# Kernel optimization log

Hardware: AMD Instinct MI355X
Metric: run time of the kernel (lower is better)

## Reference

```python
import jax, jax.numpy as jnp
import numpy as np

TEMPERATURE = 0.5
HEAD_DIM = 64
NUM_HEADS = 4

N_NODES = 50000
N_EDGES = 800000
DIM = 256


def setup_inputs() -> dict:
    key = jax.random.key(0)
    ks = jax.random.split(key, 7)
    h = jax.random.normal(ks[0], (N_NODES, DIM), dtype=jnp.float32)
    src = jax.random.randint(ks[1], (N_EDGES,), 0, N_NODES)
    dst = jax.random.randint(ks[2], (N_EDGES,), 0, N_NODES)
    attn_q = jax.random.normal(ks[3], (DIM, NUM_HEADS * HEAD_DIM), dtype=jnp.float32) * 0.02
    attn_k = jax.random.normal(ks[4], (DIM, NUM_HEADS * HEAD_DIM), dtype=jnp.float32) * 0.02
    W = jax.random.normal(ks[5], (DIM, DIM), dtype=jnp.float32) * (1.0 / np.sqrt(DIM))
    b = jnp.zeros((DIM,), dtype=jnp.float32)
    return {"h": h, "src": src, "dst": dst, "attn_q": attn_q, "attn_k": attn_k, "W": W, "b": b}


def _edge_softmax_by_dst(a, dst, n_nodes):
    # softmax over incoming edges of each destination node (DGL edge_softmax)
    m = jax.ops.segment_max(a, dst, num_segments=n_nodes)
    e = jnp.exp(a - m[dst])
    s = jax.ops.segment_sum(e, dst, num_segments=n_nodes)
    return e / s[dst]


def reference(h, src, dst, attn_q, attn_k, W, b):
    n = h.shape[0]
    v = h @ W.T + b                         # iv Linear: [N, D]
    q = h @ attn_q                          # [N, H*64]
    k = h @ attn_k                          # [N, H*64]
    # per-edge score: mean over heads then over head_dim == mean over all H*64,
    # preceded by /8 -> dot(q_src, k_dst) / (8 * H * 64)
    scale = 1.0 / (8.0 * NUM_HEADS * HEAD_DIM)
    a = jnp.einsum('ed,ed->e', q[src], k[dst]) * scale   # [E]
    # global standardization over all edges (std unbiased=False)
    m = a.mean()
    s = jnp.sqrt(((a - m) ** 2).mean())
    a = (a - m) / s / TEMPERATURE
    a = _edge_softmax_by_dst(a, dst, n)     # [E]
    # message passing: sum_{e: dst(e)=i} a_e * v[src(e)]
    out = jax.ops.segment_sum(v[src] * a[:, None], dst, num_segments=n)  # [N, D]
    return out, a
```

## Files before the change

### kernel.cpp

```cpp
#include <hip/hip_runtime.h>
#include <math.h>

#define DIM 256
#define NQKV 768
#define STAT_BLOCKS 2048

typedef float  f32x4 __attribute__((ext_vector_type(4)));
typedef short  bs8   __attribute__((ext_vector_type(8)));

__device__ __forceinline__ ushort f2bf(float f) {
    unsigned int u = __float_as_uint(f);
    u += 0x7fffu + ((u >> 16) & 1u);
    return (ushort)(u >> 16);
}
__device__ __forceinline__ float bf2f(ushort u) {
    return __uint_as_float(((unsigned int)u) << 16);
}

#define MFMA16(c, a, b) \
    asm("s_nop 1\n\tv_mfma_f32_16x16x32_bf16 %0, %1, %2, %0" : "+v"(c) : "v"(a), "v"(b))

__global__ __launch_bounds__(256) void conv_h(
    const float* __restrict__ h, ushort* __restrict__ h_bf, int total8)
{
    const int idx = blockIdx.x * 256 + threadIdx.x;
    if (idx >= total8) return;
    const float4* hp = (const float4*)(h + (size_t)idx * 8);
    float4 a = hp[0], b = hp[1];
    uint4 o;
    o.x = (unsigned)f2bf(a.x) | ((unsigned)f2bf(a.y) << 16);
    o.y = (unsigned)f2bf(a.z) | ((unsigned)f2bf(a.w) << 16);
    o.z = (unsigned)f2bf(b.x) | ((unsigned)f2bf(b.y) << 16);
    o.w = (unsigned)f2bf(b.z) | ((unsigned)f2bf(b.w) << 16);
    *(uint4*)(h_bf + (size_t)idx * 8) = o;
}

__global__ __launch_bounds__(256) void build_bt(
    const float* __restrict__ attn_q, const float* __restrict__ attn_k,
    const float* __restrict__ W, ushort* __restrict__ bt)
{
    const int n = blockIdx.x;
    const int k = threadIdx.x;
    float val;
    if (n < 256)      val = attn_q[(size_t)k * 256 + n];
    else if (n < 512) val = attn_k[(size_t)k * 256 + (n - 256)];
    else              val = W[(size_t)(n - 512) * 256 + k];
    bt[(size_t)n * 256 + k] = f2bf(val);
}

__global__ __launch_bounds__(256) void gemm_qkv_mfma(
    const ushort* __restrict__ h_bf, const ushort* __restrict__ bt,
    const float* __restrict__ bias, ushort* __restrict__ qkv, int M)
{
    __shared__ __align__(16) ushort As[128 * 40];
    __shared__ __align__(16) ushort Bs[128 * 40];

    const int bm = blockIdx.x * 128;
    const int bn = blockIdx.y * 128;
    const int t    = threadIdx.x;
    const int lane = t & 63;
    const int wid  = t >> 6;
    const int wm   = wid >> 1;
    const int wn   = wid & 1;
    const int fr   = lane & 15;
    const int ko   = (lane >> 4) * 8;

    f32x4 acc[4][4];
    #pragma unroll
    for (int i = 0; i < 4; ++i)
        #pragma unroll
        for (int j = 0; j < 4; ++j)
            acc[i][j] = (f32x4){0.f, 0.f, 0.f, 0.f};

    for (int k0 = 0; k0 < DIM; k0 += 32) {
        #pragma unroll
        for (int ii = 0; ii < 2; ++ii) {
            const int s   = t * 2 + ii;
            const int row = s >> 2;
            const int sl  = s & 3;
            int ga = bm + row; if (ga > M - 1) ga = M - 1;
            uint4 va = *(const uint4*)(h_bf + (size_t)ga * 256 + k0 + sl * 8);
            *(uint4*)(As + row * 40 + sl * 8) = va;
            uint4 vb = *(const uint4*)(bt + (size_t)(bn + row) * 256 + k0 + sl * 8);
            *(uint4*)(Bs + row * 40 + sl * 8) = vb;
        }
        __syncthreads();

        bs8 af[4], bf_[4];
        #pragma unroll
        for (int f = 0; f < 4; ++f) {
            af[f]  = *(const bs8*)(As + (wm * 64 + f * 16 + fr) * 40 + ko);
            bf_[f] = *(const bs8*)(Bs + (wn * 64 + f * 16 + fr) * 40 + ko);
        }
        #pragma unroll
        for (int fm = 0; fm < 4; ++fm)
            #pragma unroll
            for (int fn = 0; fn < 4; ++fn)
                MFMA16(acc[fm][fn], af[fm], bf_[fn]);

        __syncthreads();
    }

    asm volatile("s_nop 7\n\ts_nop 7\n\ts_nop 7" ::: );

    #pragma unroll
    for (int fm = 0; fm < 4; ++fm) {
        const int rowbase = bm + wm * 64 + fm * 16 + (lane >> 4) * 4;
        #pragma unroll
        for (int fn = 0; fn < 4; ++fn) {
            const int col = bn + wn * 64 + fn * 16 + fr;
            float bv = (col >= 512) ? bias[col - 512] : 0.f;
            #pragma unroll
            for (int r = 0; r < 4; ++r) {
                const int row = rowbase + r;
                if (row < M)
                    qkv[(size_t)row * NQKV + col] = f2bf(acc[fm][fn][r] + bv);
            }
        }
    }
}

__global__ __launch_bounds__(256) void deg_count(
    const int* __restrict__ dst, int* __restrict__ deg, int E)
{
    const int e = blockIdx.x * 256 + threadIdx.x;
    if (e < E) atomicAdd(&deg[dst[e]], 1);
}

__global__ __launch_bounds__(1024) void scan_rowptr(
    const int* __restrict__ deg, int* __restrict__ row_ptr, int N)
{
    const int tid  = threadIdx.x;
    const int lane = tid & 63;
    const int wv   = tid >> 6;

    if (tid == 0) row_ptr[0] = 0;

    __shared__ int woff[17];
    __shared__ int carryS;
    if (tid == 0) carryS = 0;
    __syncthreads();

    for (int base = 0; base < N; base += 4096) {
        int x[4], pre[4];
        int run = 0;
        #pragma unroll
        for (int j = 0; j < 4; ++j) {
            const int i = base + tid * 4 + j;
            const int v = (i < N) ? deg[i] : 0;
            pre[j] = run; x[j] = v; run += v;
        }
        int incl = run;
        #pragma unroll
        for (int off = 1; off < 64; off <<= 1) {
            int y = __shfl_up(incl, off);
            if (lane >= off) incl += y;
        }
        const int wex = incl - run;
        if (lane == 63) woff[wv] = incl;
        __syncthreads();
        if (wv == 0) {
            int wtot = (lane < 16) ? woff[lane] : 0;
            int winc = wtot;
            #pragma unroll
            for (int off = 1; off < 16; off <<= 1) {
                int y = __shfl_up(winc, off);
                if (lane >= off) winc += y;
            }
            if (lane < 16) woff[lane] = winc - wtot;
            if (lane == 15) woff[16] = winc;
        }
        __syncthreads();
        const int basev = carryS + woff[wv] + wex;
        #pragma unroll
        for (int j = 0; j < 4; ++j) {
            const int i = base + tid * 4 + j;
            if (i < N) row_ptr[i + 1] = basev + pre[j] + x[j];
        }
        __syncthreads();
        if (tid == 0) carryS += woff[16];
        __syncthreads();
    }
}

__global__ __launch_bounds__(256) void scatter_edges(
    const int* __restrict__ src, const int* __restrict__ dst,
    const int* __restrict__ row_ptr, int* __restrict__ cursor,
    int4* __restrict__ edata, int E)
{
    const int e = blockIdx.x * 256 + threadIdx.x;
    if (e < E) {
        const int d = dst[e];
        const int pos = row_ptr[d] + atomicAdd(&cursor[d], 1);
        edata[pos] = make_int4(src[e], d, e, 0);
    }
}

__global__ __launch_bounds__(256) void edge_dot_csr(
    const ushort* __restrict__ qkv, const int4* __restrict__ edata,
    float* __restrict__ a_rawc, double* __restrict__ partials, int E)
{
    const int lane = threadIdx.x & 63;
    const int wid  = threadIdx.x >> 6;
    const int w    = blockIdx.x * 4 + wid;
    const int nw   = gridDim.x * 4;
    const int chunk = (E + nw - 1) / nw;
    const int p0 = w * chunk;
    const int p1 = min(E, p0 + chunk);

    double lsum = 0.0, lsum2 = 0.0;
    int p = p0;
    for (; p + 2 <= p1; p += 2) {
        const int4 e0 = edata[p];
        const int4 e1 = edata[p + 1];
        ushort4 qa0 = *(const ushort4*)(qkv + (size_t)e0.x * NQKV + lane * 4);
        ushort4 kb0 = *(const ushort4*)(qkv + (size_t)e0.y * NQKV + 256 + lane * 4);
        ushort4 qa1 = *(const ushort4*)(qkv + (size_t)e1.x * NQKV + lane * 4);
        ushort4 kb1 = *(const ushort4*)(qkv + (size_t)e1.y * NQKV + 256 + lane * 4);
        float d0 = bf2f(qa0.x) * bf2f(kb0.x) + bf2f(qa0.y) * bf2f(kb0.y)
                 + bf2f(qa0.z) * bf2f(kb0.z) + bf2f(qa0.w) * bf2f(kb0.w);
        float d1 = bf2f(qa1.x) * bf2f(kb1.x) + bf2f(qa1.y) * bf2f(kb1.y)
                 + bf2f(qa1.z) * bf2f(kb1.z) + bf2f(qa1.w) * bf2f(kb1.w);
        #pragma unroll
        for (int off = 32; off; off >>= 1) {
            d0 += __shfl_xor(d0, off);
            d1 += __shfl_xor(d1, off);
        }
        if (lane == 0) {
            a_rawc[p]     = d0;
            a_rawc[p + 1] = d1;
            lsum  += (double)d0 + (double)d1;
            lsum2 += (double)d0 * (double)d0 + (double)d1 * (double)d1;
        }
    }
    if (p < p1) {
        const int4 e0 = edata[p];
        ushort4 qa0 = *(const ushort4*)(qkv + (size_t)e0.x * NQKV + lane * 4);
        ushort4 kb0 = *(const ushort4*)(qkv + (size_t)e0.y * NQKV + 256 + lane * 4);
        float d0 = bf2f(qa0.x) * bf2f(kb0.x) + bf2f(qa0.y) * bf2f(kb0.y)
                 + bf2f(qa0.z) * bf2f(kb0.z) + bf2f(qa0.w) * bf2f(kb0.w);
        #pragma unroll
        for (int off = 32; off; off >>= 1) d0 += __shfl_xor(d0, off);
        if (lane == 0) {
            a_rawc[p] = d0;
            lsum  += (double)d0;
            lsum2 += (double)d0 * (double)d0;
        }
    }

    __shared__ double bsum[4], bsum2[4];
    if (lane == 0) { bsum[wid] = lsum; bsum2[wid] = lsum2; }
    __syncthreads();
    if (threadIdx.x == 0) {
        partials[blockIdx.x]             = bsum[0] + bsum[1] + bsum[2] + bsum[3];
        partials[gridDim.x + blockIdx.x] = bsum2[0] + bsum2[1] + bsum2[2] + bsum2[3];
    }
}

__global__ __launch_bounds__(256) void finalize_coef(
    const double* __restrict__ partials, float* __restrict__ coef, int E)
{
    __shared__ double red[256];
    const int tid = threadIdx.x;
    double s1 = 0.0, s2 = 0.0;
    for (int i = tid; i < STAT_BLOCKS; i += 256) {
        s1 += partials[i];
        s2 += partials[STAT_BLOCKS + i];
    }
    red[tid] = s1;
    __syncthreads();
    for (int off = 128; off; off >>= 1) {
        if (tid < off) red[tid] += red[tid + off];
        __syncthreads();
    }
    const double tot1 = red[0];
    __syncthreads();
    red[tid] = s2;
    __syncthreads();
    for (int off = 128; off; off >>= 1) {
        if (tid < off) red[tid] += red[tid + off];
        __syncthreads();
    }
    if (tid == 0) {
        const double mean = tot1 / (double)E;
        const double var  = red[0] / (double)E - mean * mean;
        coef[0] = (float)mean;
        coef[1] = (float)(1.0 / (sqrt(var) * 0.5));
    }
}

__global__ __launch_bounds__(256) void agg_fused(
    const ushort* __restrict__ qkv, const float* __restrict__ a_rawc,
    const int4* __restrict__ edata, const int* __restrict__ row_ptr,
    const float* __restrict__ coef,
    float* __restrict__ out, float* __restrict__ a_out, int N)
{
    const int node = blockIdx.x;
    const int tid  = threadIdx.x;
    const int lane = tid & 63;
    const int wv   = tid >> 6;
    const int s  = row_ptr[node];
    const int en = row_ptr[node + 1];
    const float mean = coef[0];
    const float mul  = coef[1];

    float lsum = 0.f;
    for (int j = s + tid; j < en; j += 256)
        lsum += __expf((a_rawc[j] - mean) * mul);
    #pragma unroll
    for (int off = 32; off; off >>= 1) lsum += __shfl_xor(lsum, off);
    __shared__ float ws4[4];
    if (lane == 0) ws4[wv] = lsum;
    __syncthreads();
    const float rcp = 1.0f / (ws4[0] + ws4[1] + ws4[2] + ws4[3]);

    __shared__ float ae[64];
    __shared__ int   asrc[64];
    float acc = 0.f;
    for (int base = s; base < en; base += 64) {
        const int cnt = min(64, en - base);
        __syncthreads();
        if (tid < cnt) {
            const int4 ed = edata[base + tid];
            const float wgt = __expf((a_rawc[base + tid] - mean) * mul) * rcp;
            ae[tid]   = wgt;
            asrc[tid] = ed.x;
            a_out[ed.z] = wgt;
        }
        __syncthreads();
        #pragma unroll 4
        for (int j = 0; j < cnt; ++j)
            acc += ae[j] * bf2f(qkv[(size_t)asrc[j] * NQKV + 512 + tid]);
    }
    out[(size_t)node * DIM + tid] = acc;
}

extern "C" void kernel_launch(void* const* d_in, const int* in_sizes, int n_in,
                              void* d_out, int out_size, void* d_ws, size_t ws_size,
                              hipStream_t stream)
{
    const float* h      = (const float*)d_in[0];
    const int*   src    = (const int*)d_in[1];
    const int*   dst    = (const int*)d_in[2];
    const float* attn_q = (const float*)d_in[3];
    const float* attn_k = (const float*)d_in[4];
    const float* W      = (const float*)d_in[5];
    const float* bias   = (const float*)d_in[6];

    const int N = in_sizes[0] / DIM;
    const int E = in_sizes[1];

    float* out   = (float*)d_out;
    float* a_out = out + (size_t)N * DIM;

    char* ws = (char*)d_ws;
    ushort* h_bf  = (ushort*)ws;
    int4*   edata = (int4*)ws;
    ws += (size_t)N * DIM * 2;
    ushort* qkv   = (ushort*)ws; ws += (size_t)N * NQKV * 2;
    ushort* bt    = (ushort*)ws; ws += (size_t)NQKV * DIM * 2;
    float* a_rawc = (float*)ws;  ws += (size_t)E * 4;
    int* deg      = (int*)ws;    ws += (size_t)N * 4;
    int* cursor   = (int*)ws;    ws += (size_t)N * 4;
    double* partials = (double*)ws; ws += (size_t)STAT_BLOCKS * 2 * 8;
    float* coef   = (float*)ws;  ws += 8;
    int* row_ptr  = (int*)ws;    ws += (size_t)(N + 1) * 4;

    hipMemsetAsync(deg,    0, (size_t)N * 4, stream);
    hipMemsetAsync(cursor, 0, (size_t)N * 4, stream);

    const int total8 = N * DIM / 8;
    conv_h<<<(total8 + 255) / 256, 256, 0, stream>>>(h, h_bf, total8);
    build_bt<<<NQKV, 256, 0, stream>>>(attn_q, attn_k, W, bt);

    dim3 gg((N + 127) / 128, NQKV / 128);
    gemm_qkv_mfma<<<gg, 256, 0, stream>>>(h_bf, bt, bias, qkv, N);

    deg_count<<<(E + 255) / 256, 256, 0, stream>>>(dst, deg, E);
    scan_rowptr<<<1, 1024, 0, stream>>>(deg, row_ptr, N);
    scatter_edges<<<(E + 255) / 256, 256, 0, stream>>>(src, dst, row_ptr, cursor, edata, E);
    edge_dot_csr<<<STAT_BLOCKS, 256, 0, stream>>>(qkv, edata, a_rawc, partials, E);
    finalize_coef<<<1, 256, 0, stream>>>(partials, coef, E);
    agg_fused<<<N, 256, 0, stream>>>(qkv, a_rawc, edata, row_ptr, coef, out, a_out, N);
}
```

Baseline: 485.4 us.

## Widen edge-dot gathers to two edges per wave and split aggregation across waves

The edge dot-product kernel now processes two edges per wavefront, with each 32-lane half-wave doing 16-byte loads. It unrolls to eight edges per iteration to keep more gathers in flight. The aggregation kernel drops the LDS-staged, barrier-synchronised 64-edge batches: each of the four waves handles every fourth edge, gathers a full 256-wide bf16 value row with 8-byte per-lane loads, and the four partial sums are combined through LDS at the end. The aim is fewer instructions per gathered byte, more memory-level parallelism and fewer barriers, at the cost of more registers and an extra LDS reduction.

New measurement: 461.9 us. 1.05x faster.

```diff
diff --git a/kernel.cpp b/kernel.cpp
--- a/kernel.cpp
+++ b/kernel.cpp
@@ -15,6 +15,14 @@
 }
 __device__ __forceinline__ float bf2f(ushort u) {
     return __uint_as_float(((unsigned int)u) << 16);
+}
+__device__ __forceinline__ float dotu4(uint4 a, uint4 b) {
+    float s;
+    s  = bf2f((ushort)a.x) * bf2f((ushort)b.x) + bf2f((ushort)(a.x >> 16)) * bf2f((ushort)(b.x >> 16));
+    s += bf2f((ushort)a.y) * bf2f((ushort)b.y) + bf2f((ushort)(a.y >> 16)) * bf2f((ushort)(b.y >> 16));
+    s += bf2f((ushort)a.z) * bf2f((ushort)b.z) + bf2f((ushort)(a.z >> 16)) * bf2f((ushort)(b.z >> 16));
+    s += bf2f((ushort)a.w) * bf2f((ushort)b.w) + bf2f((ushort)(a.w >> 16)) * bf2f((ushort)(b.w >> 16));
+    return s;
 }
 
 #define MFMA16(c, a, b) \
@@ -202,51 +210,80 @@
 {
     const int lane = threadIdx.x & 63;
     const int wid  = threadIdx.x >> 6;
+    const int lq   = lane & 31;
+    const int hh   = lane >> 5;
     const int w    = blockIdx.x * 4 + wid;
     const int nw   = gridDim.x * 4;
     const int chunk = (E + nw - 1) / nw;
-    const int p0 = w * chunk;
+    const int p0 = min(E, w * chunk);
     const int p1 = min(E, p0 + chunk);
 
     double lsum = 0.0, lsum2 = 0.0;
     int p = p0;
-    for (; p + 2 <= p1; p += 2) {
-        const int4 e0 = edata[p];
-        const int4 e1 = edata[p + 1];
-        ushort4 qa0 = *(const ushort4*)(qkv + (size_t)e0.x * NQKV + lane * 4);
-        ushort4 kb0 = *(const ushort4*)(qkv + (size_t)e0.y * NQKV + 256 + lane * 4);
-        ushort4 qa1 = *(const ushort4*)(qkv + (size_t)e1.x * NQKV + lane * 4);
-        ushort4 kb1 = *(const ushort4*)(qkv + (size_t)e1.y * NQKV + 256 + lane * 4);
-        float d0 = bf2f(qa0.x) * bf2f(kb0.x) + bf2f(qa0.y) * bf2f(kb0.y)
-                 + bf2f(qa0.z) * bf2f(kb0.z) + bf2f(qa0.w) * bf2f(kb0.w);
-        float d1 = bf2f(qa1.x) * bf2f(kb1.x) + bf2f(qa1.y) * bf2f(kb1.y)
-                 + bf2f(qa1.z) * bf2f(kb1.z) + bf2f(qa1.w) * bf2f(kb1.w);
-        #pragma unroll
-        for (int off = 32; off; off >>= 1) {
+
+    for (; p + 8 <= p1; p += 8) {
+        const int4 ed0 = edata[p     + hh];
+        const int4 ed1 = edata[p + 2 + hh];
+        const int4 ed2 = edata[p + 4 + hh];
+        const int4 ed3 = edata[p + 6 + hh];
+        uint4 q0 = *(const uint4*)(qkv + (size_t)ed0.x * NQKV + lq * 8);
+        uint4 q1 = *(const uint4*)(qkv + (size_t)ed1.x * NQKV + lq * 8);
+        uint4 q2 = *(const uint4*)(qkv + (size_t)ed2.x * NQKV + lq * 8);
+        uint4 q3 = *(const uint4*)(qkv + (size_t)ed3.x * NQKV + lq * 8);
+        uint4 k0 = *(const uint4*)(qkv + (size_t)ed0.y * NQKV + 256 + lq * 8);
+        uint4 k1 = *(const uint4*)(qkv + (size_t)ed1.y * NQKV + 256 + lq * 8);
+        uint4 k2 = *(const uint4*)(qkv + (size_t)ed2.y * NQKV + 256 + lq * 8);
+        uint4 k3 = *(const uint4*)(qkv + (size_t)ed3.y * NQKV + 256 + lq * 8);
+        float d0 = dotu4(q0, k0);
+        float d1 = dotu4(q1, k1);
+        float d2 = dotu4(q2, k2);
+        float d3 = dotu4(q3, k3);
+        #pragma unroll
+        for (int off = 16; off; off >>= 1) {
             d0 += __shfl_xor(d0, off);
             d1 += __shfl_xor(d1, off);
-        }
-        if (lane == 0) {
-            a_rawc[p]     = d0;
-            a_rawc[p + 1] = d1;
-            lsum  += (double)d0 + (double)d1;
-            lsum2 += (double)d0 * (double)d0 + (double)d1 * (double)d1;
+            d2 += __shfl_xor(d2, off);
+            d3 += __shfl_xor(d3, off);
+        }
+        if (lq == 0) {
+            a_rawc[p     + hh] = d0;
+            a_rawc[p + 2 + hh] = d1;
+            a_rawc[p + 4 + hh] = d2;
+            a_rawc[p + 6 + hh] = d3;
+            lsum  += (double)d0 + (double)d1 + (double)d2 + (double)d3;
+            lsum2 += (double)d0 * d0 + (double)d1 * d1
+                   + (double)d2 * d2 + (double)d3 * d3;
+        }
+    }
+    for (; p + 2 <= p1; p += 2) {
+        const int4 ed0 = edata[p + hh];
+        uint4 q0 = *(const uint4*)(qkv + (size_t)ed0.x * NQKV + lq * 8);
+        uint4 k0 = *(const uint4*)(qkv + (size_t)ed0.y * NQKV + 256 + lq * 8);
+        float d0 = dotu4(q0, k0);
+        #pragma unroll
+        for (int off = 16; off; off >>= 1) d0 += __shfl_xor(d0, off);
+        if (lq == 0) {
+            a_rawc[p + hh] = d0;
+            lsum  += (double)d0;
+            lsum2 += (double)d0 * d0;
         }
     }
     if (p < p1) {
-        const int4 e0 = edata[p];
-        ushort4 qa0 = *(const ushort4*)(qkv + (size_t)e0.x * NQKV + lane * 4);
-        ushort4 kb0 = *(const ushort4*)(qkv + (size_t)e0.y * NQKV + 256 + lane * 4);
-        float d0 = bf2f(qa0.x) * bf2f(kb0.x) + bf2f(qa0.y) * bf2f(kb0.y)
-                 + bf2f(qa0.z) * bf2f(kb0.z) + bf2f(qa0.w) * bf2f(kb0.w);
-        #pragma unroll
-        for (int off = 32; off; off >>= 1) d0 += __shfl_xor(d0, off);
+        const int4 ed0 = edata[p];
+        uint4 q0 = *(const uint4*)(qkv + (size_t)ed0.x * NQKV + lq * 8);
+        uint4 k0 = *(const uint4*)(qkv + (size_t)ed0.y * NQKV + 256 + lq * 8);
+        float d0 = dotu4(q0, k0);
+        #pragma unroll
+        for (int off = 16; off; off >>= 1) d0 += __shfl_xor(d0, off);
         if (lane == 0) {
             a_rawc[p] = d0;
             lsum  += (double)d0;
-            lsum2 += (double)d0 * (double)d0;
-        }
-    }
+            lsum2 += (double)d0 * d0;
+        }
+    }
+
+    lsum  += __shfl_xor(lsum, 32);
+    lsum2 += __shfl_xor(lsum2, 32);
 
     __shared__ double bsum[4], bsum2[4];
     if (lane == 0) { bsum[wid] = lsum; bsum2[wid] = lsum2; }
@@ -314,25 +351,37 @@
     __syncthreads();
     const float rcp = 1.0f / (ws4[0] + ws4[1] + ws4[2] + ws4[3]);
 
-    __shared__ float ae[64];
-    __shared__ int   asrc[64];
-    float acc = 0.f;
-    for (int base = s; base < en; base += 64) {
-        const int cnt = min(64, en - base);
-        __syncthreads();
-        if (tid < cnt) {
-            const int4 ed = edata[base + tid];
-            const float wgt = __expf((a_rawc[base + tid] - mean) * mul) * rcp;
-            ae[tid]   = wgt;
-            asrc[tid] = ed.x;
-            a_out[ed.z] = wgt;
-        }
-        __syncthreads();
-        #pragma unroll 4
-        for (int j = 0; j < cnt; ++j)
-            acc += ae[j] * bf2f(qkv[(size_t)asrc[j] * NQKV + 512 + tid]);
-    }
-    out[(size_t)node * DIM + tid] = acc;
+    float4 acc = make_float4(0.f, 0.f, 0.f, 0.f);
+    int j = s + wv;
+    for (; j + 4 < en; j += 8) {
+        const int4 edA = edata[j];
+        const int4 edB = edata[j + 4];
+        const float wA = __expf((a_rawc[j]     - mean) * mul) * rcp;
+        const float wB = __expf((a_rawc[j + 4] - mean) * mul) * rcp;
+        ushort4 vA = *(const ushort4*)(qkv + (size_t)edA.x * NQKV + 512 + lane * 4);
+        ushort4 vB = *(const ushort4*)(qkv + (size_t)edB.x * NQKV + 512 + lane * 4);
+        if (lane == 0) { a_out[edA.z] = wA; a_out[edB.z] = wB; }
+        acc.x += wA * bf2f(vA.x) + wB * bf2f(vB.x);
+        acc.y += wA * bf2f(vA.y) + wB * bf2f(vB.y);
+        acc.z += wA * bf2f(vA.z) + wB * bf2f(vB.z);
+        acc.w += wA * bf2f(vA.w) + wB * bf2f(vB.w);
+    }
+    if (j < en) {
+        const int4 edA = edata[j];
+        const float wA = __expf((a_rawc[j] - mean) * mul) * rcp;
+        ushort4 vA = *(const ushort4*)(qkv + (size_t)edA.x * NQKV + 512 + lane * 4);
+        if (lane == 0) a_out[edA.z] = wA;
+        acc.x += wA * bf2f(vA.x);
+        acc.y += wA * bf2f(vA.y);
+        acc.z += wA * bf2f(vA.z);
+        acc.w += wA * bf2f(vA.w);
+    }
+
+    __shared__ float lds[4][DIM];
+    *(float4*)&lds[wv][lane * 4] = acc;
+    __syncthreads();
+    out[(size_t)node * DIM + tid] =
+        lds[0][tid] + lds[1][tid] + lds[2][tid] + lds[3][tid];
 }
 
 extern "C" void kernel_launch(void* const* d_in, const int* in_sizes, int n_in,
```
